# Performance work log

Hardware: AMD Instinct MI355X
Metric: run time of the kernel (lower is better)

Reference implementation:

```python
import jax, jax.numpy as jnp
import numpy as np

EPS = 1e-5

def _bn_eval(x, gamma, beta, mean, var):
    return (x - mean) * (gamma / jnp.sqrt(var + EPS)) + beta

def setup_inputs() -> dict:
    key = jax.random.key(0)
    ks = jax.random.split(key, 12)
    N, E, D, C, H = 100000, 1000000, 64, 32, 128
    fused = 4 * D + C  # 288
    z = jax.random.normal(ks[0], (N, D), dtype=jnp.float32)
    edge_index = jax.random.randint(ks[1], (2, E), 0, N, dtype=jnp.int64)
    edge_context = jax.random.normal(ks[2], (E, C), dtype=jnp.float32)
    W1 = jax.random.normal(ks[3], (fused, H), dtype=jnp.float32) / np.sqrt(fused)
    b1 = jnp.zeros((H,), jnp.float32)
    g1 = jnp.ones((H,), jnp.float32); be1 = jnp.zeros((H,), jnp.float32)
    m1 = jnp.zeros((H,), jnp.float32); v1 = jnp.ones((H,), jnp.float32)
    W2 = jax.random.normal(ks[4], (H, H // 2), dtype=jnp.float32) / np.sqrt(H)
    b2 = jnp.zeros((H // 2,), jnp.float32)
    g2 = jnp.ones((H // 2,), jnp.float32); be2 = jnp.zeros((H // 2,), jnp.float32)
    m2 = jnp.zeros((H // 2,), jnp.float32); v2 = jnp.ones((H // 2,), jnp.float32)
    W3 = jax.random.normal(ks[5], (H // 2, 1), dtype=jnp.float32) / np.sqrt(H // 2)
    b3 = jnp.zeros((1,), jnp.float32)
    return {"z": z, "edge_index": edge_index, "edge_context": edge_context,
            "W1": W1, "b1": b1, "g1": g1, "be1": be1, "m1": m1, "v1": v1,
            "W2": W2, "b2": b2, "g2": g2, "be2": be2, "m2": m2, "v2": v2,
            "W3": W3, "b3": b3}

def reference(z, edge_index, edge_context,
              W1, b1, g1, be1, m1, v1,
              W2, b2, g2, be2, m2, v2,
              W3, b3):
    # gather endpoint embeddings: [E, D]
    src = z[edge_index[0]]
    dst = z[edge_index[1]]
    # fused features: [E, 4*D + C]
    fused = jnp.concatenate([src, dst, src * dst, jnp.abs(src - dst), edge_context], axis=1)
    x = jax.nn.relu(_bn_eval(fused @ W1 + b1, g1, be1, m1, v1))
    x = jax.nn.relu(_bn_eval(x @ W2 + b2, g2, be2, m2, v2))
    return (x @ W3 + b3).reshape(-1)
```

## Files before the change

kernel.cpp:

```cpp
#include <hip/hip_runtime.h>
#include <hip/hip_bf16.h>

typedef __attribute__((ext_vector_type(8))) short bf16x8;
typedef __attribute__((ext_vector_type(4))) float f32x4;
typedef __attribute__((ext_vector_type(4))) unsigned int u32x4;
typedef __attribute__((ext_vector_type(2))) unsigned int u32x2;

#define EPS 1e-5f

__device__ inline unsigned short f2bf(float x) {
  unsigned int u = __builtin_bit_cast(unsigned int, x);
  unsigned int r = (u + 0x7FFFu + ((u >> 16) & 1u)) >> 16;
  return (unsigned short)r;
}

__device__ inline unsigned int pk2(float a, float b) {
  return (unsigned int)f2bf(a) | ((unsigned int)f2bf(b) << 16);
}

__global__ void prep_kernel(const float* __restrict__ W1, const float* __restrict__ W2,
                            const float* __restrict__ b1, const float* __restrict__ g1,
                            const float* __restrict__ be1, const float* __restrict__ m1,
                            const float* __restrict__ v1,
                            const float* __restrict__ b2, const float* __restrict__ g2,
                            const float* __restrict__ be2, const float* __restrict__ m2,
                            const float* __restrict__ v2,
                            unsigned short* __restrict__ w1f, unsigned short* __restrict__ w2f,
                            float* __restrict__ sc) {
  int t = blockIdx.x * 256 + threadIdx.x;
  if (t < 36864) {
    int j = t & 7, l = (t >> 3) & 63, f = t >> 9;
    int kb = f >> 3, nb = f & 7;
    int rk = kb * 32 + ((l >> 4) << 3) + j;
    int cn = (nb << 4) + (l & 15);
    w1f[t] = f2bf(W1[rk * 128 + cn]);
  } else if (t < 45056) {
    int o = t - 36864;
    int j = o & 7, l = (o >> 3) & 63, f = o >> 9;
    int kb = f >> 2, nb = f & 3;
    int rk = kb * 32 + ((l >> 4) << 3) + j;
    int cn = (nb << 4) + (l & 15);
    w2f[o] = f2bf(W2[rk * 64 + cn]);
  } else if (t < 45184) {
    int j = t - 45056;
    float s = g1[j] * rsqrtf(v1[j] + EPS);
    sc[j] = s;
    sc[128 + j] = (b1[j] - m1[j]) * s + be1[j];
  } else if (t < 45248) {
    int j = t - 45184;
    float s = g2[j] * rsqrtf(v2[j] + EPS);
    sc[256 + j] = s;
    sc[320 + j] = (b2[j] - m2[j]) * s + be2[j];
  }
}

#define LDS_SC_OFF 73728
#define LDS_A_OFF 75776
#define LDS_TOTAL (75776 + 81920)

__global__ __launch_bounds__(1024, 4) void fused_kernel(
    const float* __restrict__ z, const int* __restrict__ ei, const float* __restrict__ ctx,
    const unsigned short* __restrict__ w1f, const unsigned short* __restrict__ w2f,
    const float* __restrict__ sc, const float* __restrict__ w3, const float* __restrict__ b3,
    float* __restrict__ out, int E, int nblk) {
  extern __shared__ char lds[];
  char* W1B = lds;
  float* SC = (float*)(lds + LDS_SC_OFF);
  char* AR = lds + LDS_A_OFF;

  const int tid = threadIdx.x;
  {
    const f32x4* s = (const f32x4*)w1f;
    f32x4* d = (f32x4*)W1B;
#pragma unroll
    for (int i = 0; i < 4; i++) d[i * 1024 + tid] = s[i * 1024 + tid];
    if (tid < 512) d[4096 + tid] = s[4096 + tid];
    if (tid < 128) {
      SC[tid] = sc[tid];
      SC[128 + tid] = sc[128 + tid];
    } else if (tid < 192) {
      int j = tid - 128;
      SC[256 + j] = sc[256 + j];
      SC[320 + j] = sc[320 + j];
      SC[384 + j] = w3[j];
    } else if (tid == 192) {
      SC[448] = b3[0];
    }
  }

  const int lane = tid & 63, wave = tid >> 6;
  const int g = lane >> 4, lq = lane & 15;
  const int wr = wave >> 2, wc = wave & 3;
  const int w2r = wave >> 1, w2c = wave & 1;
  const int sr = tid >> 3, sh = tid & 7;
  const int grid = gridDim.x;

  int t = blockIdx.x;
  f32x4 sv0, sv1, dv0, dv1, cv;
  int i0n, i1n;
  {
    int e = (t << 7) + sr;
    int es = e < E ? e : E - 1;
    int a0 = ei[es], a1 = ei[E + es];
    cv = *(const f32x4*)(ctx + (size_t)es * 32 + sh * 4);
    const f32x4* zs = (const f32x4*)(z + ((size_t)a0 * 64 + sh * 8));
    sv0 = zs[0]; sv1 = zs[1];
    const f32x4* zd = (const f32x4*)(z + ((size_t)a1 * 64 + sh * 8));
    dv0 = zd[0]; dv1 = zd[1];
    int tn = t + grid; if (tn >= nblk) tn = t;
    int en = (tn << 7) + sr;
    int esn = en < E ? en : E - 1;
    i0n = ei[esn]; i1n = ei[E + esn];
  }
  __syncthreads();

  for (; t < nblk; t += grid) {
    {
      const int rswz = (sr & 7) << 4;
      char* rowp = AR + sr * 640;
      u32x4 ps = {pk2(sv0[0], sv0[1]), pk2(sv0[2], sv0[3]), pk2(sv1[0], sv1[1]), pk2(sv1[2], sv1[3])};
      u32x4 pd = {pk2(dv0[0], dv0[1]), pk2(dv0[2], dv0[3]), pk2(dv1[0], dv1[1]), pk2(dv1[2], dv1[3])};
      u32x4 pp = {pk2(sv0[0] * dv0[0], sv0[1] * dv0[1]), pk2(sv0[2] * dv0[2], sv0[3] * dv0[3]),
                  pk2(sv1[0] * dv1[0], sv1[1] * dv1[1]), pk2(sv1[2] * dv1[2], sv1[3] * dv1[3])};
      u32x4 pa = {pk2(fabsf(sv0[0] - dv0[0]), fabsf(sv0[1] - dv0[1])),
                  pk2(fabsf(sv0[2] - dv0[2]), fabsf(sv0[3] - dv0[3])),
                  pk2(fabsf(sv1[0] - dv1[0]), fabsf(sv1[1] - dv1[1])),
                  pk2(fabsf(sv1[2] - dv1[2]), fabsf(sv1[3] - dv1[3]))};
      u32x2 pc = {pk2(cv[0], cv[1]), pk2(cv[2], cv[3])};
      *(u32x4*)(rowp + ((sh * 16) ^ rswz)) = ps;
      *(u32x4*)(rowp + ((128 + sh * 16) ^ rswz)) = pd;
      *(u32x4*)(rowp + ((256 + sh * 16) ^ rswz)) = pp;
      *(u32x4*)(rowp + ((384 + sh * 16) ^ rswz)) = pa;
      *(u32x2*)(rowp + 512 + ((sh * 8) ^ rswz)) = pc;
    }
    {
      int tn = t + grid; if (tn >= nblk) tn = t;
      const f32x4* zs = (const f32x4*)(z + ((size_t)i0n * 64 + sh * 8));
      sv0 = zs[0]; sv1 = zs[1];
      const f32x4* zd = (const f32x4*)(z + ((size_t)i1n * 64 + sh * 8));
      dv0 = zd[0]; dv1 = zd[1];
      int en = (tn << 7) + sr;
      int esn = en < E ? en : E - 1;
      cv = *(const f32x4*)(ctx + (size_t)esn * 32 + sh * 4);
      int tn2 = tn + grid; if (tn2 >= nblk) tn2 = tn;
      int en2 = (tn2 << 7) + sr;
      int esn2 = en2 < E ? en2 : E - 1;
      i0n = ei[esn2]; i1n = ei[E + esn2];
    }
    __syncthreads();

    f32x4 acc[2][2];
#pragma unroll
    for (int mf = 0; mf < 2; mf++)
#pragma unroll
      for (int nf = 0; nf < 2; nf++) {
        f32x4 zv = {0.f, 0.f, 0.f, 0.f};
        acc[mf][nf] = zv;
      }
    const bf16x8* W1F = (const bf16x8*)W1B;
#pragma unroll
    for (int kb = 0; kb < 9; kb++) {
      bf16x8 a[2], b[2];
#pragma unroll
      for (int mf = 0; mf < 2; mf++) {
        int row = wr * 32 + mf * 16 + lq;
        a[mf] = *(const bf16x8*)(AR + row * 640 + ((kb * 64 + g * 16) ^ ((row & 7) << 4)));
      }
#pragma unroll
      for (int nf = 0; nf < 2; nf++) b[nf] = W1F[(kb * 8 + wc * 2 + nf) * 64 + lane];
#pragma unroll
      for (int mf = 0; mf < 2; mf++)
#pragma unroll
        for (int nf = 0; nf < 2; nf++)
          acc[mf][nf] = __builtin_amdgcn_mfma_f32_16x16x32_bf16(a[mf], b[nf], acc[mf][nf], 0, 0, 0);
    }
    __syncthreads();

    ((f32x4*)(AR + 32768))[tid] = ((const f32x4*)w2f)[tid];
#pragma unroll
    for (int nf = 0; nf < 2; nf++) {
      const int col = wc * 32 + nf * 16 + lq;
      const float s1v = SC[col], c1v = SC[128 + col];
#pragma unroll
      for (int mf = 0; mf < 2; mf++) {
#pragma unroll
        for (int j = 0; j < 4; j++) {
          int row = wr * 32 + mf * 16 + 4 * g + j;
          float v = fmaxf(acc[mf][nf][j] * s1v + c1v, 0.f);
          *(unsigned short*)(AR + row * 256 + ((col * 2) ^ ((row & 7) << 4))) = f2bf(v);
        }
      }
    }
    __syncthreads();

    f32x4 acc2[2];
#pragma unroll
    for (int nf = 0; nf < 2; nf++) {
      f32x4 zv = {0.f, 0.f, 0.f, 0.f};
      acc2[nf] = zv;
    }
    const bf16x8* W2F = (const bf16x8*)(AR + 32768);
#pragma unroll
    for (int kb = 0; kb < 4; kb++) {
      int row = w2r * 16 + lq;
      bf16x8 a2 = *(const bf16x8*)(AR + row * 256 + ((kb * 64 + g * 16) ^ ((row & 7) << 4)));
      bf16x8 b2[2];
#pragma unroll
      for (int nf = 0; nf < 2; nf++) b2[nf] = W2F[(kb * 4 + w2c * 2 + nf) * 64 + lane];
#pragma unroll
      for (int nf = 0; nf < 2; nf++)
        acc2[nf] = __builtin_amdgcn_mfma_f32_16x16x32_bf16(a2, b2[nf], acc2[nf], 0, 0, 0);
    }

    float* l3 = (float*)(AR + 49152);
    const int colA = w2c * 32 + lq, colB = colA + 16;
    const float s2A = SC[256 + colA], c2A = SC[320 + colA];
    const float s2B = SC[256 + colB], c2B = SC[320 + colB];
    const float w3A = SC[384 + colA], w3B = SC[384 + colB];
#pragma unroll
    for (int j = 0; j < 4; j++) {
      float vA = fmaxf(acc2[0][j] * s2A + c2A, 0.f);
      float vB = fmaxf(acc2[1][j] * s2B + c2B, 0.f);
      float p = vA * w3A + vB * w3B;
      p += __shfl_xor(p, 1);
      p += __shfl_xor(p, 2);
      p += __shfl_xor(p, 4);
      p += __shfl_xor(p, 8);
      if (lq == 0) l3[(w2r * 16 + 4 * g + j) * 2 + w2c] = p;
    }
    __syncthreads();
    if (tid < 128) {
      int e = (t << 7) + tid;
      if (e < E) out[e] = l3[tid * 2] + l3[tid * 2 + 1] + SC[448];
    }
    __syncthreads();
  }
}

extern "C" void kernel_launch(void* const* d_in, const int* in_sizes, int n_in,
                              void* d_out, int out_size, void* d_ws, size_t ws_size,
                              hipStream_t stream) {
  const float* z = (const float*)d_in[0];
  const int* ei = (const int*)d_in[1];
  const float* ctx = (const float*)d_in[2];
  const float* W1 = (const float*)d_in[3];
  const float* b1 = (const float*)d_in[4];
  const float* g1 = (const float*)d_in[5];
  const float* be1 = (const float*)d_in[6];
  const float* m1 = (const float*)d_in[7];
  const float* v1 = (const float*)d_in[8];
  const float* W2 = (const float*)d_in[9];
  const float* b2 = (const float*)d_in[10];
  const float* g2 = (const float*)d_in[11];
  const float* be2 = (const float*)d_in[12];
  const float* m2 = (const float*)d_in[13];
  const float* v2 = (const float*)d_in[14];
  const float* W3 = (const float*)d_in[15];
  const float* b3 = (const float*)d_in[16];
  float* out = (float*)d_out;
  const int E = out_size;

  unsigned short* w1f = (unsigned short*)d_ws;
  unsigned short* w2f = (unsigned short*)((char*)d_ws + 73728);
  float* sc = (float*)((char*)d_ws + 90112);

  prep_kernel<<<177, 256, 0, stream>>>(W1, W2, b1, g1, be1, m1, v1,
                                       b2, g2, be2, m2, v2, w1f, w2f, sc);

  const int nblk = (E + 127) >> 7;
  (void)hipFuncSetAttribute((const void*)fused_kernel,
                            hipFuncAttributeMaxDynamicSharedMemorySize, LDS_TOTAL);
  fused_kernel<<<256, 1024, LDS_TOTAL, stream>>>(z, ei, ctx, w1f, w2f, sc, W3, b3,
                                                 out, E, nblk);
}
```

Baseline: 162.9 us.

## Keep W1/W2 fragments in registers and overlap A-tile write with layer-2 stage

Holds the first four K-blocks of W1 and all of W2 in registers, so only part of W1 stays in LDS and the per-iteration W2 copy into LDS goes away. Layer-1 output moves to a separate LDS buffer, which lets the next tile's fused-feature write and gather run between layer 1 and layer 2. This removes one barrier per iteration. The cost is higher register pressure under 1024-thread launch bounds, with a risk of spills.

```diff
diff --git a/kernel.cpp b/kernel.cpp
--- a/kernel.cpp
+++ b/kernel.cpp
@@ -54,9 +54,11 @@
   }
 }
 
-#define LDS_SC_OFF 73728
-#define LDS_A_OFF 75776
-#define LDS_TOTAL (75776 + 81920)
+#define LDS_SC_OFF 40960
+#define LDS_A_OFF 43008
+#define LDS_X1_OFF 124928
+#define LDS_L3_OFF 157696
+#define LDS_TOTAL 158720
 
 __global__ __launch_bounds__(1024, 4) void fused_kernel(
     const float* __restrict__ z, const int* __restrict__ ei, const float* __restrict__ ctx,
@@ -64,17 +66,26 @@
     const float* __restrict__ sc, const float* __restrict__ w3, const float* __restrict__ b3,
     float* __restrict__ out, int E, int nblk) {
   extern __shared__ char lds[];
-  char* W1B = lds;
+  char* W1L = lds;
   float* SC = (float*)(lds + LDS_SC_OFF);
   char* AR = lds + LDS_A_OFF;
+  char* X1 = lds + LDS_X1_OFF;
+  float* l3 = (float*)(lds + LDS_L3_OFF);
 
   const int tid = threadIdx.x;
+  const int lane = tid & 63, wave = tid >> 6;
+  const int g = lane >> 4, lq = lane & 15;
+  const int wr = wave >> 2, wc = wave & 3;
+  const int w2r = wave >> 1, w2c = wave & 1;
+  const int sr = tid >> 3, sh = tid & 7;
+  const int grid = gridDim.x;
+
   {
-    const f32x4* s = (const f32x4*)w1f;
-    f32x4* d = (f32x4*)W1B;
-#pragma unroll
-    for (int i = 0; i < 4; i++) d[i * 1024 + tid] = s[i * 1024 + tid];
-    if (tid < 512) d[4096 + tid] = s[4096 + tid];
+    const f32x4* s = (const f32x4*)(w1f + 16384);
+    f32x4* d = (f32x4*)W1L;
+    d[tid] = s[tid];
+    d[1024 + tid] = s[1024 + tid];
+    if (tid < 512) d[2048 + tid] = s[2048 + tid];
     if (tid < 128) {
       SC[tid] = sc[tid];
       SC[128 + tid] = sc[128 + tid];
@@ -88,16 +99,55 @@
     }
   }
 
-  const int lane = tid & 63, wave = tid >> 6;
-  const int g = lane >> 4, lq = lane & 15;
-  const int wr = wave >> 2, wc = wave & 3;
-  const int w2r = wave >> 1, w2c = wave & 1;
-  const int sr = tid >> 3, sh = tid & 7;
-  const int grid = gridDim.x;
-
-  int t = blockIdx.x;
+  bf16x8 w1r[4][2], w2g[4][2];
+  {
+    const bf16x8* W1G = (const bf16x8*)w1f;
+    const bf16x8* W2G = (const bf16x8*)w2f;
+#pragma unroll
+    for (int kb = 0; kb < 4; kb++)
+#pragma unroll
+      for (int nf = 0; nf < 2; nf++) {
+        w1r[kb][nf] = W1G[(kb * 8 + wc * 2 + nf) * 64 + lane];
+        w2g[kb][nf] = W2G[(kb * 4 + w2c * 2 + nf) * 64 + lane];
+      }
+  }
+
   f32x4 sv0, sv1, dv0, dv1, cv;
   int i0n, i1n;
+  int t = blockIdx.x;
+
+  auto writeA = [&]() {
+    const int rswz = (sr & 7) << 4;
+    char* rowp = AR + sr * 640;
+    u32x4 ps = {pk2(sv0[0], sv0[1]), pk2(sv0[2], sv0[3]), pk2(sv1[0], sv1[1]), pk2(sv1[2], sv1[3])};
+    u32x4 pd = {pk2(dv0[0], dv0[1]), pk2(dv0[2], dv0[3]), pk2(dv1[0], dv1[1]), pk2(dv1[2], dv1[3])};
+    u32x4 pp = {pk2(sv0[0] * dv0[0], sv0[1] * dv0[1]), pk2(sv0[2] * dv0[2], sv0[3] * dv0[3]),
+                pk2(sv1[0] * dv1[0], sv1[1] * dv1[1]), pk2(sv1[2] * dv1[2], sv1[3] * dv1[3])};
+    u32x4 pa = {pk2(fabsf(sv0[0] - dv0[0]), fabsf(sv0[1] - dv0[1])),
+                pk2(fabsf(sv0[2] - dv0[2]), fabsf(sv0[3] - dv0[3])),
+                pk2(fabsf(sv1[0] - dv1[0]), fabsf(sv1[1] - dv1[1])),
+                pk2(fabsf(sv1[2] - dv1[2]), fabsf(sv1[3] - dv1[3]))};
+    u32x2 pc = {pk2(cv[0], cv[1]), pk2(cv[2], cv[3])};
+    *(u32x4*)(rowp + ((sh * 16) ^ rswz)) = ps;
+    *(u32x4*)(rowp + ((128 + sh * 16) ^ rswz)) = pd;
+    *(u32x4*)(rowp + ((256 + sh * 16) ^ rswz)) = pp;
+    *(u32x4*)(rowp + ((384 + sh * 16) ^ rswz)) = pa;
+    *(u32x2*)(rowp + 512 + ((sh * 8) ^ rswz)) = pc;
+  };
+  auto gatherNext = [&](int tg) {
+    const f32x4* zs = (const f32x4*)(z + ((size_t)i0n * 64 + sh * 8));
+    sv0 = zs[0]; sv1 = zs[1];
+    const f32x4* zd = (const f32x4*)(z + ((size_t)i1n * 64 + sh * 8));
+    dv0 = zd[0]; dv1 = zd[1];
+    int eg = (tg << 7) + sr;
+    int esg = eg < E ? eg : E - 1;
+    cv = *(const f32x4*)(ctx + (size_t)esg * 32 + sh * 4);
+    int tn = tg + grid; if (tn >= nblk) tn = tg;
+    int en = (tn << 7) + sr;
+    int esn = en < E ? en : E - 1;
+    i0n = ei[esn]; i1n = ei[E + esn];
+  };
+
   {
     int e = (t << 7) + sr;
     int es = e < E ? e : E - 1;
@@ -112,43 +162,14 @@
     int esn = en < E ? en : E - 1;
     i0n = ei[esn]; i1n = ei[E + esn];
   }
+  writeA();
+  {
+    int tn = t + grid; if (tn >= nblk) tn = t;
+    gatherNext(tn);
+  }
   __syncthreads();
 
   for (; t < nblk; t += grid) {
-    {
-      const int rswz = (sr & 7) << 4;
-      char* rowp = AR + sr * 640;
-      u32x4 ps = {pk2(sv0[0], sv0[1]), pk2(sv0[2], sv0[3]), pk2(sv1[0], sv1[1]), pk2(sv1[2], sv1[3])};
-      u32x4 pd = {pk2(dv0[0], dv0[1]), pk2(dv0[2], dv0[3]), pk2(dv1[0], dv1[1]), pk2(dv1[2], dv1[3])};
-      u32x4 pp = {pk2(sv0[0] * dv0[0], sv0[1] * dv0[1]), pk2(sv0[2] * dv0[2], sv0[3] * dv0[3]),
-                  pk2(sv1[0] * dv1[0], sv1[1] * dv1[1]), pk2(sv1[2] * dv1[2], sv1[3] * dv1[3])};
-      u32x4 pa = {pk2(fabsf(sv0[0] - dv0[0]), fabsf(sv0[1] - dv0[1])),
-                  pk2(fabsf(sv0[2] - dv0[2]), fabsf(sv0[3] - dv0[3])),
-                  pk2(fabsf(sv1[0] - dv1[0]), fabsf(sv1[1] - dv1[1])),
-                  pk2(fabsf(sv1[2] - dv1[2]), fabsf(sv1[3] - dv1[3]))};
-      u32x2 pc = {pk2(cv[0], cv[1]), pk2(cv[2], cv[3])};
-      *(u32x4*)(rowp + ((sh * 16) ^ rswz)) = ps;
-      *(u32x4*)(rowp + ((128 + sh * 16) ^ rswz)) = pd;
-      *(u32x4*)(rowp + ((256 + sh * 16) ^ rswz)) = pp;
-      *(u32x4*)(rowp + ((384 + sh * 16) ^ rswz)) = pa;
-      *(u32x2*)(rowp + 512 + ((sh * 8) ^ rswz)) = pc;
-    }
-    {
-      int tn = t + grid; if (tn >= nblk) tn = t;
-      const f32x4* zs = (const f32x4*)(z + ((size_t)i0n * 64 + sh * 8));
-      sv0 = zs[0]; sv1 = zs[1];
-      const f32x4* zd = (const f32x4*)(z + ((size_t)i1n * 64 + sh * 8));
-      dv0 = zd[0]; dv1 = zd[1];
-      int en = (tn << 7) + sr;
-      int esn = en < E ? en : E - 1;
-      cv = *(const f32x4*)(ctx + (size_t)esn * 32 + sh * 4);
-      int tn2 = tn + grid; if (tn2 >= nblk) tn2 = tn;
-      int en2 = (tn2 << 7) + sr;
-      int esn2 = en2 < E ? en2 : E - 1;
-      i0n = ei[esn2]; i1n = ei[E + esn2];
-    }
-    __syncthreads();
-
     f32x4 acc[2][2];
 #pragma unroll
     for (int mf = 0; mf < 2; mf++)
@@ -157,7 +178,7 @@
         f32x4 zv = {0.f, 0.f, 0.f, 0.f};
         acc[mf][nf] = zv;
       }
-    const bf16x8* W1F = (const bf16x8*)W1B;
+    const bf16x8* W1F = (const bf16x8*)W1L;
 #pragma unroll
     for (int kb = 0; kb < 9; kb++) {
       bf16x8 a[2], b[2];
@@ -166,8 +187,14 @@
         int row = wr * 32 + mf * 16 + lq;
         a[mf] = *(const bf16x8*)(AR + row * 640 + ((kb * 64 + g * 16) ^ ((row & 7) << 4)));
       }
-#pragma unroll
-      for (int nf = 0; nf < 2; nf++) b[nf] = W1F[(kb * 8 + wc * 2 + nf) * 64 + lane];
+      if (kb < 4) {
+        b[0] = w1r[kb][0];
+        b[1] = w1r[kb][1];
+      } else {
+#pragma unroll
+        for (int nf = 0; nf < 2; nf++)
+          b[nf] = W1F[((kb - 4) * 8 + wc * 2 + nf) * 64 + lane];
+      }
 #pragma unroll
       for (int mf = 0; mf < 2; mf++)
 #pragma unroll
@@ -176,7 +203,6 @@
     }
     __syncthreads();
 
-    ((f32x4*)(AR + 32768))[tid] = ((const f32x4*)w2f)[tid];
 #pragma unroll
     for (int nf = 0; nf < 2; nf++) {
       const int col = wc * 32 + nf * 16 + lq;
@@ -187,9 +213,15 @@
         for (int j = 0; j < 4; j++) {
           int row = wr * 32 + mf * 16 + 4 * g + j;
           float v = fmaxf(acc[mf][nf][j] * s1v + c1v, 0.f);
-          *(unsigned short*)(AR + row * 256 + ((col * 2) ^ ((row & 7) << 4))) = f2bf(v);
+          *(unsigned short*)(X1 + row * 256 + ((col * 2) ^ ((row & 7) << 4))) = f2bf(v);
         }
       }
+    }
+    writeA();
+    {
+      int tn2 = t + 2 * grid;
+      if (tn2 >= nblk) tn2 = t + grid < nblk ? t + grid : t;
+      gatherNext(tn2);
     }
     __syncthreads();
 
@@ -199,20 +231,15 @@
       f32x4 zv = {0.f, 0.f, 0.f, 0.f};
       acc2[nf] = zv;
     }
-    const bf16x8* W2F = (const bf16x8*)(AR + 32768);
 #pragma unroll
     for (int kb = 0; kb < 4; kb++) {
       int row = w2r * 16 + lq;
-      bf16x8 a2 = *(const bf16x8*)(AR + row * 256 + ((kb * 64 + g * 16) ^ ((row & 7) << 4)));
-      bf16x8 b2[2];
-#pragma unroll
-      for (int nf = 0; nf < 2; nf++) b2[nf] = W2F[(kb * 4 + w2c * 2 + nf) * 64 + lane];
+      bf16x8 a2 = *(const bf16x8*)(X1 + row * 256 + ((kb * 64 + g * 16) ^ ((row & 7) << 4)));
 #pragma unroll
       for (int nf = 0; nf < 2; nf++)
-        acc2[nf] = __builtin_amdgcn_mfma_f32_16x16x32_bf16(a2, b2[nf], acc2[nf], 0, 0, 0);
-    }
-
-    float* l3 = (float*)(AR + 49152);
+        acc2[nf] = __builtin_amdgcn_mfma_f32_16x16x32_bf16(a2, w2g[kb][nf], acc2[nf], 0, 0, 0);
+    }
+
     const int colA = w2c * 32 + lq, colB = colA + 16;
     const float s2A = SC[256 + colA], c2A = SC[320 + colA];
     const float s2B = SC[256 + colB], c2B = SC[320 + colB];
@@ -229,11 +256,11 @@
       if (lq == 0) l3[(w2r * 16 + 4 * g + j) * 2 + w2c] = p;
     }
     __syncthreads();
+
     if (tid < 128) {
       int e = (t << 7) + tid;
       if (e < E) out[e] = l3[tid * 2] + l3[tid * 2 + 1] + SC[448];
     }
-    __syncthreads();
   }
 }
 
```

Result: slower. 413.8 us (+154.0%).
